# Performance work log

Hardware: AMD Instinct MI355X
Metric: run time of the kernel (lower is better)

## Reference

```python
import jax, jax.numpy as jnp
import numpy as np

B, T, I, H = 2048, 2048, 9, 16


def setup_inputs() -> dict:
    key = jax.random.key(0)
    ks = jax.random.split(key, 8)
    s = 1.0 / np.sqrt(H)  # PyTorch default uniform init bound
    x = jax.random.normal(ks[0], (B, T, I), dtype=jnp.float32)
    x_lens = jax.random.randint(ks[1], (B,), 1, T + 1)  # lengths in [1, T]
    W_ih = jax.random.uniform(ks[2], (4 * H, I), jnp.float32, -s, s)
    W_hh = jax.random.uniform(ks[3], (4 * H, H), jnp.float32, -s, s)
    b_ih = jax.random.uniform(ks[4], (4 * H,), jnp.float32, -s, s)
    b_hh = jax.random.uniform(ks[5], (4 * H,), jnp.float32, -s, s)
    W_lin = jax.random.uniform(ks[6], (2, H), jnp.float32, -s, s)
    b_lin = jax.random.uniform(ks[7], (2,), jnp.float32, -s, s)
    return {"x": x, "x_lens": x_lens, "W_ih": W_ih, "W_hh": W_hh,
            "b_ih": b_ih, "b_hh": b_hh, "W_lin": W_lin, "b_lin": b_lin}


def reference(x, x_lens, W_ih, W_hh, b_ih, b_hh, W_lin, b_lin):
    # x: [B, T, I]; single-layer LSTM (PyTorch gate order i, f, g, o)
    b = b_ih + b_hh
    xT = jnp.swapaxes(x, 0, 1)                       # [T, B, I]
    x_proj = jnp.einsum('tbi,gi->tbg', xT, W_ih) + b  # input projection, precomputed
    h0 = jnp.zeros((x.shape[0], W_hh.shape[1]), x.dtype)

    def step(carry, xp):
        h, c = carry
        gates = xp + h @ W_hh.T                      # [B, 4H]
        i, f, g, o = jnp.split(gates, 4, axis=-1)
        i = jax.nn.sigmoid(i)
        f = jax.nn.sigmoid(f)
        g = jnp.tanh(g)
        o = jax.nn.sigmoid(o)
        c = f * c + i * g
        h = o * jnp.tanh(c)
        return (h, c), h

    (_, _), hs = jax.lax.scan(step, (h0, h0), x_proj)  # hs: [T, B, H]
    # lstm_out[arange(B), x_lens - 1] with time-major layout:
    hidden = hs[x_lens - 1, jnp.arange(x.shape[0])]    # [B, H]
    return hidden @ W_lin.T + b_lin                    # [B, 2]
```

## Files before the change

kernel.cpp:

```cpp
#include <hip/hip_runtime.h>

static constexpr int B_ = 2048;
static constexpr int T_ = 2048;
static constexpr int I_ = 9;
static constexpr int H_ = 16;

__device__ __forceinline__ float f_exp2(float x) {
#if __has_builtin(__builtin_amdgcn_exp2f)
  return __builtin_amdgcn_exp2f(x);
#else
  float r; asm volatile("v_exp_f32 %0, %1" : "=v"(r) : "v"(x)); return r;
#endif
}
__device__ __forceinline__ float f_rcp(float x) {
#if __has_builtin(__builtin_amdgcn_rcpf)
  return __builtin_amdgcn_rcpf(x);
#else
  float r; asm volatile("v_rcp_f32 %0, %1" : "=v"(r) : "v"(x)); return r;
#endif
}

__device__ __forceinline__ float rlane(float v, int lane) {
  return __builtin_bit_cast(float,
      __builtin_amdgcn_readlane(__builtin_bit_cast(int, v), lane));
}

template <int SEL>
__device__ __forceinline__ float quad_bcast(float v) {
  constexpr int ctrl = SEL * 0x55;
  return __builtin_bit_cast(float, __builtin_amdgcn_update_dpp(
      0, __builtin_bit_cast(int, v), ctrl, 0xF, 0xF, true));
}

__global__ __launch_bounds__(256, 1) void ParityLSTM_kernel(
    const float* __restrict__ x, const int* __restrict__ x_lens,
    const float* __restrict__ W_ih, const float* __restrict__ W_hh,
    const float* __restrict__ b_ih, const float* __restrict__ b_hh,
    const float* __restrict__ W_lin, const float* __restrict__ b_lin,
    float* __restrict__ out) {
  const int lane = threadIdx.x & 63;
  const int wave = threadIdx.x >> 6;
  const int b = blockIdx.x * 4 + wave;

  const int q = lane & 3;
  const int m = lane >> 2;
  const int g_id = q * H_ + m;

  const bool isG = (q == 2);
  constexpr float kT = -2.8853900817779268f;
  constexpr float kS = -1.4426950408889634f;
  const float sc1 = isG ? kT : kS;
  const float m2 = isG ? (2.0f * kT) : 1.0f;
  const float a2 = isG ? (-kT) : 0.0f;

  float whh[H_];
#pragma unroll
  for (int k = 0; k < H_; ++k) whh[k] = W_hh[g_id * H_ + k] * sc1;
  float wih[I_];
#pragma unroll
  for (int k = 0; k < I_; ++k) wih[k] = W_ih[g_id * I_ + k] * sc1;
  const float bias = (b_ih[g_id] + b_hh[g_id]) * sc1;

  const int len = __builtin_amdgcn_readfirstlane(x_lens[b]);

  float cs = 0.0f, h = 0.0f;
  const float* xb = x + (size_t)b * T_ * I_;

  float xr[I_];
  {
    const float* xp = xb + (size_t)lane * I_;
#pragma unroll
    for (int k = 0; k < I_; ++k) xr[k] = xp[k];
  }

  for (int t0 = 0; t0 < len; t0 += 64) {
    float xn[I_];
    const bool more = (t0 + 64) < len;
    if (more) {
      const float* xp = xb + (size_t)(t0 + 64 + lane) * I_;
#pragma unroll
      for (int k = 0; k < I_; ++k) xn[k] = xp[k];
    }
    const int ns = min(64, len - t0);
#pragma unroll 4
    for (int s = 0; s < ns; ++s) {
      float acc[4] = {bias, 0.0f, 0.0f, 0.0f};
#pragma unroll
      for (int k = 0; k < I_; ++k)
        acc[k & 3] = fmaf(rlane(xr[k], s), wih[k], acc[k & 3]);
#pragma unroll
      for (int k = 0; k < H_; ++k)
        acc[k & 3] = fmaf(rlane(h, 4 * k), whh[k], acc[k & 3]);
      const float a = (acc[0] + acc[1]) + (acc[2] + acc[3]);

      const float e = f_exp2(a);
      const float r = f_rcp(1.0f + e);
      const float act = fmaf(m2, r, a2);

      const float iv = quad_bcast<0>(act);
      const float gv = quad_bcast<2>(act);
      const float fv = quad_bcast<1>(act);
      const float ov = quad_bcast<3>(act);

      cs = fmaf(fv, cs, iv * gv);
      const float e2 = f_exp2(cs);
      const float th = fmaf(2.0f, f_rcp(1.0f + e2), -1.0f);
      h = ov * th;
    }
    if (more) {
#pragma unroll
      for (int k = 0; k < I_; ++k) xr[k] = xn[k];
    }
  }

  const float wl = (q < 2) ? W_lin[q * H_ + m] : 0.0f;
  float p = h * wl;
  p += __shfl_xor(p, 4, 64);
  p += __shfl_xor(p, 8, 64);
  p += __shfl_xor(p, 16, 64);
  p += __shfl_xor(p, 32, 64);
  if (lane < 2) out[2 * b + lane] = p + b_lin[lane];
}

extern "C" void kernel_launch(void* const* d_in, const int* in_sizes, int n_in,
                              void* d_out, int out_size, void* d_ws,
                              size_t ws_size, hipStream_t stream) {
  const float* x = (const float*)d_in[0];
  const int* x_lens = (const int*)d_in[1];
  const float* W_ih = (const float*)d_in[2];
  const float* W_hh = (const float*)d_in[3];
  const float* b_ih = (const float*)d_in[4];
  const float* b_hh = (const float*)d_in[5];
  const float* W_lin = (const float*)d_in[6];
  const float* b_lin = (const float*)d_in[7];
  float* out = (float*)d_out;

  dim3 grid(B_ / 4);
  dim3 block(256);
  ParityLSTM_kernel<<<grid, block, 0, stream>>>(x, x_lens, W_ih, W_hh, b_ih,
                                                b_hh, W_lin, b_lin, out);
}
```

Measured before the change: 683.3 us.

## Interleave two batch sequences per wave to hide recurrent step latency

```diff
diff --git a/kernel.cpp b/kernel.cpp
--- a/kernel.cpp
+++ b/kernel.cpp
@@ -19,12 +19,10 @@
   float r; asm volatile("v_rcp_f32 %0, %1" : "=v"(r) : "v"(x)); return r;
 #endif
 }
-
-__device__ __forceinline__ float rlane(float v, int lane) {
+__device__ __forceinline__ float rlane(float v, int l) {
   return __builtin_bit_cast(float,
-      __builtin_amdgcn_readlane(__builtin_bit_cast(int, v), lane));
-}
-
+      __builtin_amdgcn_readlane(__builtin_bit_cast(int, v), l));
+}
 template <int SEL>
 __device__ __forceinline__ float quad_bcast(float v) {
   constexpr int ctrl = SEL * 0x55;
@@ -32,7 +30,61 @@
       0, __builtin_bit_cast(int, v), ctrl, 0xF, 0xF, true));
 }
 
-__global__ __launch_bounds__(256, 1) void ParityLSTM_kernel(
+#define PIN(v) asm("" : "+v"(v))
+
+#define DO8(M) M(0) M(1) M(2) M(3) M(4) M(5) M(6) M(7)
+
+#define PROJ9(Xp, X, sj)                                   \
+  float Xp;                                                \
+  {                                                        \
+    float p0 = fmaf(rlane(X##0, (sj)), wi0, bs);           \
+    float p1 = rlane(X##1, (sj)) * wi1;                    \
+    float p2 = rlane(X##2, (sj)) * wi2;                    \
+    p0 = fmaf(rlane(X##3, (sj)), wi3, p0);                 \
+    p1 = fmaf(rlane(X##4, (sj)), wi4, p1);                 \
+    p2 = fmaf(rlane(X##5, (sj)), wi5, p2);                 \
+    p0 = fmaf(rlane(X##6, (sj)), wi6, p0);                 \
+    p1 = fmaf(rlane(X##7, (sj)), wi7, p1);                 \
+    p2 = fmaf(rlane(X##8, (sj)), wi8, p2);                 \
+    Xp = p0 + (p1 + p2);                                   \
+  }
+
+#define LSTEP(h, cs, hf, xp, lm1, tcur)                    \
+  {                                                        \
+    float a0 = fmaf(rlane(h, 0), wh0, xp);                 \
+    float a1 = rlane(h, 4) * wh1;                          \
+    float a2 = rlane(h, 8) * wh2;                          \
+    float a3 = rlane(h, 12) * wh3;                         \
+    a0 = fmaf(rlane(h, 16), wh4, a0);                      \
+    a1 = fmaf(rlane(h, 20), wh5, a1);                      \
+    a2 = fmaf(rlane(h, 24), wh6, a2);                      \
+    a3 = fmaf(rlane(h, 28), wh7, a3);                      \
+    a0 = fmaf(rlane(h, 32), wh8, a0);                      \
+    a1 = fmaf(rlane(h, 36), wh9, a1);                      \
+    a2 = fmaf(rlane(h, 40), wh10, a2);                     \
+    a3 = fmaf(rlane(h, 44), wh11, a3);                     \
+    a0 = fmaf(rlane(h, 48), wh12, a0);                     \
+    a1 = fmaf(rlane(h, 52), wh13, a1);                     \
+    a2 = fmaf(rlane(h, 56), wh14, a2);                     \
+    a3 = fmaf(rlane(h, 60), wh15, a3);                     \
+    float aa = (a0 + a1) + (a2 + a3);                      \
+    float e = f_exp2(aa);                                  \
+    float r = f_rcp(1.0f + e);                             \
+    float act = fmaf(m2c, r, a2c);                         \
+    float iv = quad_bcast<0>(act);                         \
+    float gv = quad_bcast<2>(act);                         \
+    float fv = quad_bcast<1>(act);                         \
+    float ov = quad_bcast<3>(act);                         \
+    cs = fmaf(fv, cs, iv * gv);                            \
+    float e2 = f_exp2(cs);                                 \
+    float r2 = f_rcp(1.0f + e2);                           \
+    h = fmaf(ov + ov, r2, -ov);                            \
+    hf = ((tcur) == (lm1)) ? h : hf;                       \
+  }
+
+__global__ __launch_bounds__(256)
+__attribute__((amdgpu_waves_per_eu(1, 1)))
+void ParityLSTM_kernel(
     const float* __restrict__ x, const int* __restrict__ x_lens,
     const float* __restrict__ W_ih, const float* __restrict__ W_hh,
     const float* __restrict__ b_ih, const float* __restrict__ b_hh,
@@ -40,86 +92,101 @@
     float* __restrict__ out) {
   const int lane = threadIdx.x & 63;
   const int wave = threadIdx.x >> 6;
-  const int b = blockIdx.x * 4 + wave;
+  const int wg = blockIdx.x * 4 + wave;
+  const int bA = 2 * wg;
+  const int bB = 2 * wg + 1;
 
   const int q = lane & 3;
   const int m = lane >> 2;
   const int g_id = q * H_ + m;
 
-  const bool isG = (q == 2);
   constexpr float kT = -2.8853900817779268f;
   constexpr float kS = -1.4426950408889634f;
+  const bool isG = (q == 2);
   const float sc1 = isG ? kT : kS;
-  const float m2 = isG ? (2.0f * kT) : 1.0f;
-  const float a2 = isG ? (-kT) : 0.0f;
-
-  float whh[H_];
-#pragma unroll
-  for (int k = 0; k < H_; ++k) whh[k] = W_hh[g_id * H_ + k] * sc1;
-  float wih[I_];
-#pragma unroll
-  for (int k = 0; k < I_; ++k) wih[k] = W_ih[g_id * I_ + k] * sc1;
-  const float bias = (b_ih[g_id] + b_hh[g_id]) * sc1;
-
-  const int len = __builtin_amdgcn_readfirstlane(x_lens[b]);
-
-  float cs = 0.0f, h = 0.0f;
-  const float* xb = x + (size_t)b * T_ * I_;
-
-  float xr[I_];
-  {
-    const float* xp = xb + (size_t)lane * I_;
-#pragma unroll
-    for (int k = 0; k < I_; ++k) xr[k] = xp[k];
-  }
-
-  for (int t0 = 0; t0 < len; t0 += 64) {
-    float xn[I_];
-    const bool more = (t0 + 64) < len;
-    if (more) {
-      const float* xp = xb + (size_t)(t0 + 64 + lane) * I_;
-#pragma unroll
-      for (int k = 0; k < I_; ++k) xn[k] = xp[k];
+  const float m2c = isG ? (2.0f * kT) : 1.0f;
+  const float a2c = isG ? (-kT) : 0.0f;
+
+#define LDWH(k) float wh##k = W_hh[g_id * H_ + k] * sc1;
+  LDWH(0) LDWH(1) LDWH(2) LDWH(3) LDWH(4) LDWH(5) LDWH(6) LDWH(7)
+  LDWH(8) LDWH(9) LDWH(10) LDWH(11) LDWH(12) LDWH(13) LDWH(14) LDWH(15)
+#define LDWI(k) float wi##k = W_ih[g_id * I_ + k] * sc1;
+  LDWI(0) LDWI(1) LDWI(2) LDWI(3) LDWI(4) LDWI(5) LDWI(6) LDWI(7) LDWI(8)
+  float bs = (b_ih[g_id] + b_hh[g_id]) * sc1;
+#define PINWH(k) PIN(wh##k);
+  PINWH(0) PINWH(1) PINWH(2) PINWH(3) PINWH(4) PINWH(5) PINWH(6) PINWH(7)
+  PINWH(8) PINWH(9) PINWH(10) PINWH(11) PINWH(12) PINWH(13) PINWH(14) PINWH(15)
+#define PINWI(k) PIN(wi##k);
+  PINWI(0) PINWI(1) PINWI(2) PINWI(3) PINWI(4) PINWI(5) PINWI(6) PINWI(7)
+  PINWI(8)
+  PIN(bs);
+
+  const int lA1 = __builtin_amdgcn_readfirstlane(x_lens[bA]) - 1;
+  const int lB1 = __builtin_amdgcn_readfirstlane(x_lens[bB]) - 1;
+  const int maxlen = (lA1 > lB1 ? lA1 : lB1) + 1;
+
+  const float* xbA = x + (size_t)bA * T_ * I_;
+  const float* xbB = x + (size_t)bB * T_ * I_;
+
+  float hA = 0.f, csA = 0.f, hAf = 0.f;
+  float hB = 0.f, csB = 0.f, hBf = 0.f;
+
+#define LD9(dst, p) \
+  float dst##0 = (p)[0], dst##1 = (p)[1], dst##2 = (p)[2], dst##3 = (p)[3], \
+        dst##4 = (p)[4], dst##5 = (p)[5], dst##6 = (p)[6], dst##7 = (p)[7], \
+        dst##8 = (p)[8];
+  const float* p0A = xbA + (size_t)lane * I_;
+  const float* p0B = xbB + (size_t)lane * I_;
+  LD9(xA, p0A)
+  LD9(xB, p0B)
+
+  for (int t0 = 0; t0 < maxlen; t0 += 64) {
+#define PINX(k) PIN(xA##k); PIN(xB##k);
+    PINX(0) PINX(1) PINX(2) PINX(3) PINX(4) PINX(5) PINX(6) PINX(7) PINX(8)
+    int tpf = t0 + 64 + lane;
+    if (tpf > T_ - 1) tpf = T_ - 1;
+    const float* pA = xbA + (size_t)tpf * I_;
+    const float* pB = xbB + (size_t)tpf * I_;
+    LD9(nA, pA)
+    LD9(nB, pB)
+
+#pragma unroll 1
+    for (int sb = 0; sb < 64; sb += 8) {
+#define PROJPAIR(j) PROJ9(xpA##j, xA, sb + j) PROJ9(xpB##j, xB, sb + j)
+      DO8(PROJPAIR)
+#define STEPPAIR(j)                                        \
+      {                                                    \
+        const int tc = t0 + sb + j;                        \
+        LSTEP(hA, csA, hAf, xpA##j, lA1, tc)               \
+        LSTEP(hB, csB, hBf, xpB##j, lB1, tc)               \
+      }
+      DO8(STEPPAIR)
+#undef PROJPAIR
+#undef STEPPAIR
     }
-    const int ns = min(64, len - t0);
-#pragma unroll 4
-    for (int s = 0; s < ns; ++s) {
-      float acc[4] = {bias, 0.0f, 0.0f, 0.0f};
-#pragma unroll
-      for (int k = 0; k < I_; ++k)
-        acc[k & 3] = fmaf(rlane(xr[k], s), wih[k], acc[k & 3]);
-#pragma unroll
-      for (int k = 0; k < H_; ++k)
-        acc[k & 3] = fmaf(rlane(h, 4 * k), whh[k], acc[k & 3]);
-      const float a = (acc[0] + acc[1]) + (acc[2] + acc[3]);
-
-      const float e = f_exp2(a);
-      const float r = f_rcp(1.0f + e);
-      const float act = fmaf(m2, r, a2);
-
-      const float iv = quad_bcast<0>(act);
-      const float gv = quad_bcast<2>(act);
-      const float fv = quad_bcast<1>(act);
-      const float ov = quad_bcast<3>(act);
-
-      cs = fmaf(fv, cs, iv * gv);
-      const float e2 = f_exp2(cs);
-      const float th = fmaf(2.0f, f_rcp(1.0f + e2), -1.0f);
-      h = ov * th;
-    }
-    if (more) {
-#pragma unroll
-      for (int k = 0; k < I_; ++k) xr[k] = xn[k];
-    }
+#define ROT9(a, b) \
+  a##0 = b##0; a##1 = b##1; a##2 = b##2; a##3 = b##3; a##4 = b##4; \
+  a##5 = b##5; a##6 = b##6; a##7 = b##7; a##8 = b##8;
+    ROT9(xA, nA)
+    ROT9(xB, nB)
   }
 
   const float wl = (q < 2) ? W_lin[q * H_ + m] : 0.0f;
-  float p = h * wl;
-  p += __shfl_xor(p, 4, 64);
-  p += __shfl_xor(p, 8, 64);
-  p += __shfl_xor(p, 16, 64);
-  p += __shfl_xor(p, 32, 64);
-  if (lane < 2) out[2 * b + lane] = p + b_lin[lane];
+  float pa = hAf * wl;
+  float pb = hBf * wl;
+  pa += __shfl_xor(pa, 4, 64);
+  pa += __shfl_xor(pa, 8, 64);
+  pa += __shfl_xor(pa, 16, 64);
+  pa += __shfl_xor(pa, 32, 64);
+  pb += __shfl_xor(pb, 4, 64);
+  pb += __shfl_xor(pb, 8, 64);
+  pb += __shfl_xor(pb, 16, 64);
+  pb += __shfl_xor(pb, 32, 64);
+  if (lane < 2) {
+    const float bl = b_lin[lane];
+    out[2 * bA + lane] = pa + bl;
+    out[2 * bB + lane] = pb + bl;
+  }
 }
 
 extern "C" void kernel_launch(void* const* d_in, const int* in_sizes, int n_in,
@@ -135,7 +202,7 @@
   const float* b_lin = (const float*)d_in[7];
   float* out = (float*)d_out;
 
-  dim3 grid(B_ / 4);
+  dim3 grid(B_ / 8);
   dim3 block(256);
   ParityLSTM_kernel<<<grid, block, 0, stream>>>(x, x_lens, W_ih, W_hh, b_ih,
                                                 b_hh, W_lin, b_lin, out);
```

New measurement: 729.4 us. +6.8%, slower.

## Launch one wave per block and split gate accumulation into input and hidden chains

Applied to the files above, without the earlier changes.

```diff
diff --git a/kernel.cpp b/kernel.cpp
--- a/kernel.cpp
+++ b/kernel.cpp
@@ -19,83 +19,108 @@
   float r; asm volatile("v_rcp_f32 %0, %1" : "=v"(r) : "v"(x)); return r;
 #endif
 }
-
-__device__ __forceinline__ float rlane(float v, int lane) {
+__device__ __forceinline__ float rlane(float v, int l) {
   return __builtin_bit_cast(float,
-      __builtin_amdgcn_readlane(__builtin_bit_cast(int, v), lane));
+      __builtin_amdgcn_readlane(__builtin_bit_cast(int, v), l));
 }
-
 template <int SEL>
 __device__ __forceinline__ float quad_bcast(float v) {
   constexpr int ctrl = SEL * 0x55;
   return __builtin_bit_cast(float, __builtin_amdgcn_update_dpp(
       0, __builtin_bit_cast(int, v), ctrl, 0xF, 0xF, true));
 }
+#define PIN(v) asm("" : "+v"(v))
 
-__global__ __launch_bounds__(256, 1) void ParityLSTM_kernel(
+__global__ __launch_bounds__(64, 1) void ParityLSTM_kernel(
     const float* __restrict__ x, const int* __restrict__ x_lens,
     const float* __restrict__ W_ih, const float* __restrict__ W_hh,
     const float* __restrict__ b_ih, const float* __restrict__ b_hh,
     const float* __restrict__ W_lin, const float* __restrict__ b_lin,
     float* __restrict__ out) {
   const int lane = threadIdx.x & 63;
-  const int wave = threadIdx.x >> 6;
-  const int b = blockIdx.x * 4 + wave;
+  const int b = blockIdx.x;
 
   const int q = lane & 3;
   const int m = lane >> 2;
   const int g_id = q * H_ + m;
 
-  const bool isG = (q == 2);
   constexpr float kT = -2.8853900817779268f;
   constexpr float kS = -1.4426950408889634f;
+  const bool isG = (q == 2);
   const float sc1 = isG ? kT : kS;
-  const float m2 = isG ? (2.0f * kT) : 1.0f;
-  const float a2 = isG ? (-kT) : 0.0f;
+  const float m2c = isG ? (2.0f * kT) : 1.0f;
+  const float a2c = isG ? (-kT) : 0.0f;
 
-  float whh[H_];
-#pragma unroll
-  for (int k = 0; k < H_; ++k) whh[k] = W_hh[g_id * H_ + k] * sc1;
-  float wih[I_];
-#pragma unroll
-  for (int k = 0; k < I_; ++k) wih[k] = W_ih[g_id * I_ + k] * sc1;
-  const float bias = (b_ih[g_id] + b_hh[g_id]) * sc1;
+#define LDWH(k) float wh##k = W_hh[g_id * H_ + k] * sc1;
+  LDWH(0) LDWH(1) LDWH(2) LDWH(3) LDWH(4) LDWH(5) LDWH(6) LDWH(7)
+  LDWH(8) LDWH(9) LDWH(10) LDWH(11) LDWH(12) LDWH(13) LDWH(14) LDWH(15)
+#define LDWI(k) float wi##k = W_ih[g_id * I_ + k] * sc1;
+  LDWI(0) LDWI(1) LDWI(2) LDWI(3) LDWI(4) LDWI(5) LDWI(6) LDWI(7) LDWI(8)
+  float bs = (b_ih[g_id] + b_hh[g_id]) * sc1;
+#define PINWH(k) PIN(wh##k);
+  PINWH(0) PINWH(1) PINWH(2) PINWH(3) PINWH(4) PINWH(5) PINWH(6) PINWH(7)
+  PINWH(8) PINWH(9) PINWH(10) PINWH(11) PINWH(12) PINWH(13) PINWH(14)
+  PINWH(15)
+#define PINWI(k) PIN(wi##k);
+  PINWI(0) PINWI(1) PINWI(2) PINWI(3) PINWI(4) PINWI(5) PINWI(6) PINWI(7)
+  PINWI(8)
+  PIN(bs);
 
   const int len = __builtin_amdgcn_readfirstlane(x_lens[b]);
-
-  float cs = 0.0f, h = 0.0f;
   const float* xb = x + (size_t)b * T_ * I_;
 
-  float xr[I_];
-  {
-    const float* xp = xb + (size_t)lane * I_;
-#pragma unroll
-    for (int k = 0; k < I_; ++k) xr[k] = xp[k];
-  }
+  float h = 0.0f, cs = 0.0f;
+
+#define LD9(dst, p)                                                          \
+  float dst##0 = (p)[0], dst##1 = (p)[1], dst##2 = (p)[2], dst##3 = (p)[3], \
+        dst##4 = (p)[4], dst##5 = (p)[5], dst##6 = (p)[6], dst##7 = (p)[7], \
+        dst##8 = (p)[8];
+  const float* p0 = xb + (size_t)lane * I_;
+  LD9(xc, p0)
 
   for (int t0 = 0; t0 < len; t0 += 64) {
-    float xn[I_];
+#define PINX(k) PIN(xc##k);
+    PINX(0) PINX(1) PINX(2) PINX(3) PINX(4) PINX(5) PINX(6) PINX(7) PINX(8)
     const bool more = (t0 + 64) < len;
+    float nx0, nx1, nx2, nx3, nx4, nx5, nx6, nx7, nx8;
     if (more) {
-      const float* xp = xb + (size_t)(t0 + 64 + lane) * I_;
-#pragma unroll
-      for (int k = 0; k < I_; ++k) xn[k] = xp[k];
+      const float* pn = xb + (size_t)(t0 + 64 + lane) * I_;
+      nx0 = pn[0]; nx1 = pn[1]; nx2 = pn[2]; nx3 = pn[3]; nx4 = pn[4];
+      nx5 = pn[5]; nx6 = pn[6]; nx7 = pn[7]; nx8 = pn[8];
     }
     const int ns = min(64, len - t0);
 #pragma unroll 4
     for (int s = 0; s < ns; ++s) {
-      float acc[4] = {bias, 0.0f, 0.0f, 0.0f};
-#pragma unroll
-      for (int k = 0; k < I_; ++k)
-        acc[k & 3] = fmaf(rlane(xr[k], s), wih[k], acc[k & 3]);
-#pragma unroll
-      for (int k = 0; k < H_; ++k)
-        acc[k & 3] = fmaf(rlane(h, 4 * k), whh[k], acc[k & 3]);
-      const float a = (acc[0] + acc[1]) + (acc[2] + acc[3]);
+      float ap = fmaf(rlane(xc0, s), wi0, bs);
+      ap = fmaf(rlane(xc1, s), wi1, ap);
+      ap = fmaf(rlane(xc2, s), wi2, ap);
+      ap = fmaf(rlane(xc3, s), wi3, ap);
+      ap = fmaf(rlane(xc4, s), wi4, ap);
+      ap = fmaf(rlane(xc5, s), wi5, ap);
+      ap = fmaf(rlane(xc6, s), wi6, ap);
+      ap = fmaf(rlane(xc7, s), wi7, ap);
+      ap = fmaf(rlane(xc8, s), wi8, ap);
+      float ad = rlane(h, 0) * wh0;
+      ad = fmaf(rlane(h, 4), wh1, ad);
+      ad = fmaf(rlane(h, 8), wh2, ad);
+      ad = fmaf(rlane(h, 12), wh3, ad);
+      ad = fmaf(rlane(h, 16), wh4, ad);
+      ad = fmaf(rlane(h, 20), wh5, ad);
+      ad = fmaf(rlane(h, 24), wh6, ad);
+      ad = fmaf(rlane(h, 28), wh7, ad);
+      ad = fmaf(rlane(h, 32), wh8, ad);
+      ad = fmaf(rlane(h, 36), wh9, ad);
+      ad = fmaf(rlane(h, 40), wh10, ad);
+      ad = fmaf(rlane(h, 44), wh11, ad);
+      ad = fmaf(rlane(h, 48), wh12, ad);
+      ad = fmaf(rlane(h, 52), wh13, ad);
+      ad = fmaf(rlane(h, 56), wh14, ad);
+      ad = fmaf(rlane(h, 60), wh15, ad);
+      const float aa = ap + ad;
 
-      const float e = f_exp2(a);
+      const float e = f_exp2(aa);
       const float r = f_rcp(1.0f + e);
-      const float act = fmaf(m2, r, a2);
+      const float act = fmaf(m2c, r, a2c);
 
       const float iv = quad_bcast<0>(act);
       const float gv = quad_bcast<2>(act);
@@ -104,12 +129,12 @@
 
       cs = fmaf(fv, cs, iv * gv);
       const float e2 = f_exp2(cs);
-      const float th = fmaf(2.0f, f_rcp(1.0f + e2), -1.0f);
-      h = ov * th;
+      const float r2 = f_rcp(1.0f + e2);
+      h = ov * fmaf(2.0f, r2, -1.0f);
     }
     if (more) {
-#pragma unroll
-      for (int k = 0; k < I_; ++k) xr[k] = xn[k];
+      xc0 = nx0; xc1 = nx1; xc2 = nx2; xc3 = nx3; xc4 = nx4;
+      xc5 = nx5; xc6 = nx6; xc7 = nx7; xc8 = nx8;
     }
   }
 
@@ -135,8 +160,8 @@
   const float* b_lin = (const float*)d_in[7];
   float* out = (float*)d_out;
 
-  dim3 grid(B_ / 4);
-  dim3 block(256);
+  dim3 grid(B_);
+  dim3 block(64);
   ParityLSTM_kernel<<<grid, block, 0, stream>>>(x, x_lens, W_ih, W_hh, b_ih,
                                                 b_hh, W_lin, b_lin, out);
 }
```

After: 720.1 us. 5.4% more time.
